# Kernel optimization log

Hardware: AMD Instinct MI355X
Metric: run time of the kernel (lower is better)

Reference implementation:

```python
import jax, jax.numpy as jnp
import numpy as np

# Fixed mock-config geometry
B, S, H = 8, 4096, 2048
NK, NV, DK, DV = 2, 2, 4, 4
KDIM = NK * DK          # 8
VDIM = NV * DV          # 8
CONV_DIM = 2 * KDIM + VDIM  # 24
KSZ = 4                 # causal conv kernel size
EPS = 1e-6


def setup_inputs() -> dict:
    key = jax.random.key(0)
    ks = jax.random.split(key, 7)
    scaled = lambda k, shape, fan: jax.random.normal(k, shape, jnp.float32) * (1.0 / np.sqrt(fan))
    return {
        "x": jax.random.normal(ks[0], (B, S, H), jnp.float32),
        "w_qkv": scaled(ks[1], (CONV_DIM, H), H),   # in_proj_qkv.weight
        "w_z": scaled(ks[2], (VDIM, H), H),         # in_proj_z.weight
        "w_b": scaled(ks[3], (NV, H), H),           # in_proj_b.weight
        "w_a": scaled(ks[4], (NV, H), H),           # in_proj_a.weight
        "w_out": scaled(ks[5], (H, VDIM), VDIM),    # out_proj.weight
        "conv_w": jax.random.normal(ks[6], (CONV_DIM, 1, KSZ), jnp.float32) * 0.5,  # depthwise conv weight
        "dt_bias": jnp.ones((NV,), jnp.float32),
        "A_log": jnp.log(jnp.linspace(1.0, 2.0, NV)).astype(jnp.float32),
        "norm_w": jnp.ones((DV,), jnp.float32),     # MockRMSNormGated weight
    }


def reference(x, w_qkv, w_z, w_b, w_a, w_out, conv_w, dt_bias, A_log, norm_w):
    b_, s_, _ = x.shape
    # qkv projection -> [B, C, S] for depthwise causal conv
    mixed = jnp.einsum('bsh,ch->bcs', x, w_qkv)
    # torch conv1d(padding=K-1) then [:, :, :S] == causal left-pad K-1
    conv = jax.lax.conv_general_dilated(
        mixed, conv_w, window_strides=(1,), padding=[(KSZ - 1, 0)],
        dimension_numbers=('NCH', 'OIH', 'NCH'), feature_group_count=CONV_DIM)
    mixed = jax.nn.silu(conv).transpose(0, 2, 1)  # [B, S, C]

    z = jnp.einsum('bsh,vh->bsv', x, w_z).reshape(b_, s_, NV, DV)
    bb = jnp.einsum('bsh,nh->bsn', x, w_b)  # [B, S, NV]
    aa = jnp.einsum('bsh,nh->bsn', x, w_a)  # [B, S, NV]

    query = mixed[..., :KDIM].reshape(b_, s_, NK, DK)
    key_ = mixed[..., KDIM:2 * KDIM].reshape(b_, s_, NK, DK)
    value = mixed[..., 2 * KDIM:].reshape(b_, s_, NV, DV)

    beta = jax.nn.sigmoid(bb)                                    # [B, S, NV]
    g = -jnp.exp(A_log) * jax.nn.softplus(aa + dt_bias)          # [B, S, NV], fp32
    # num_v_heads // num_k_heads == 1 -> no repeat_interleave

    # mock chunk_gated_delta_rule: value + beta * (q + k) + g
    core = value + beta[..., None] * (query + key_) + g[..., None]  # [B, S, NV, DV]

    # gated RMSNorm over head_v_dim (fp32 math)
    h = core.astype(jnp.float32)
    var = jnp.mean(h * h, axis=-1, keepdims=True)
    h = h * jax.lax.rsqrt(var + EPS) * norm_w
    h = h * jax.nn.silu(z.astype(jnp.float32))

    out = jnp.einsum('bsv,hv->bsh', h.reshape(b_, s_, VDIM), w_out)
    return out
```

## Files before the change

### kernel.cpp

```cpp
#include <hip/hip_runtime.h>
#include <math.h>
#include <cstddef>

#define BB    8
#define SS    4096
#define HH    2048
#define ROWS  (BB*SS)
#define NC    36
#define NCP   40
#define KC    32
#define XST   33
#define KSL   256

typedef float vfloat4 __attribute__((ext_vector_type(4)));

#define MIX_OFF 131072

__global__ __launch_bounds__(256) void pack_wt(
    const float* __restrict__ w_qkv, const float* __restrict__ w_z,
    const float* __restrict__ w_b,   const float* __restrict__ w_a,
    float* __restrict__ wt) {
  int idx = blockIdx.x * 256 + threadIdx.x;
  if (idx >= HH * NCP) return;
  int k = idx / NCP, c = idx - (idx / NCP) * NCP;
  float v = 0.f;
  if      (c < 24) v = w_qkv[c * HH + k];
  else if (c < 32) v = w_z[(c - 24) * HH + k];
  else if (c < 34) v = w_b[(c - 32) * HH + k];
  else if (c < 36) v = w_a[(c - 34) * HH + k];
  wt[idx] = v;
}

__global__ __launch_bounds__(512, 4) void proj36(
    const float* __restrict__ x, const float* __restrict__ wt,
    float* __restrict__ mix) {
  __shared__ float sm[8 * 64 * XST];
  const int tid  = threadIdx.x;
  const int lane = tid & 63;
  const int wv   = __builtin_amdgcn_readfirstlane(tid >> 6);
  const int r0   = blockIdx.x * 64;

  float* xs = sm + wv * 64 * XST;
  float acc[NC];
#pragma unroll
  for (int c = 0; c < NC; ++c) acc[c] = 0.f;

  const int kbase0 = wv * KSL;
  const int srow = lane >> 3;
  const int scol = (lane & 7) * 4;
  const float* xg = x + (size_t)r0 * HH + kbase0 + scol;

  float4 buf[8];
#pragma unroll
  for (int p = 0; p < 8; ++p)
    buf[p] = *(const float4*)(xg + (size_t)(p * 8 + srow) * HH);

  for (int ch = 0; ch < 8; ++ch) {
#pragma unroll
    for (int p = 0; p < 8; ++p) {
      float* dst = xs + (p * 8 + srow) * XST + scol;
      dst[0] = buf[p].x; dst[1] = buf[p].y; dst[2] = buf[p].z; dst[3] = buf[p].w;
    }
    if (ch < 7) {
      const float* xg2 = xg + (ch + 1) * KC;
#pragma unroll
      for (int p = 0; p < 8; ++p)
        buf[p] = *(const float4*)(xg2 + (size_t)(p * 8 + srow) * HH);
    }
    const float* wrow = wt + (size_t)(kbase0 + ch * KC) * NCP;
    const float* xr = xs + lane * XST;
#pragma unroll 2
    for (int k = 0; k < KC; ++k) {
      float xv = xr[k];
#pragma unroll
      for (int c = 0; c < NC; ++c)
        acc[c] = fmaf(wrow[k * NCP + c], xv, acc[c]);
    }
  }

  __syncthreads();
  const int myhalf = lane >> 5;
  const int rr = lane & 31;
  for (int half = 0; half < 2; ++half) {
    if (half) __syncthreads();
    if (myhalf == half) {
#pragma unroll
      for (int c = 0; c < NC; ++c)
        sm[(wv * 32 + rr) * 37 + c] = acc[c];
    }
    __syncthreads();
    for (int idx = tid; idx < 32 * NC; idx += 512) {
      int row = idx / NC;
      float s = 0.f;
#pragma unroll
      for (int w = 0; w < 8; ++w) s += sm[(w * 32 + row) * 37 + (idx - row * NC)];
      mix[(size_t)(r0 + half * 32) * NC + idx] = s;
    }
  }
}

__global__ __launch_bounds__(256) void fuse_out(
    const float* __restrict__ mix,  const float* __restrict__ conv_w,
    const float* __restrict__ dt_bias, const float* __restrict__ A_log,
    const float* __restrict__ norm_w,  const float* __restrict__ w_out,
    float* __restrict__ out) {
  __shared__ float m36[35 * 37];
  __shared__ float hb[32 * 8];
  const int tid = threadIdx.x;
  const int r0  = blockIdx.x * 32;

  const long base = (long)(r0 - 3) * NC;
  for (int idx = tid; idx < 35 * NC; idx += 256) {
    int row = idx / NC, c = idx - row * NC;
    long g = base + idx;
    m36[row * 37 + c] = (g >= 0) ? mix[g] : 0.f;
  }
  __syncthreads();

  if (tid < 64) {
    const int row  = tid >> 1, n = tid & 1;
    const int spos = (r0 + row) & (SS - 1);
    float cv[12];
#pragma unroll
    for (int j = 0; j < 12; ++j) {
      int c = (j >> 2) * 8 + n * 4 + (j & 3);
      float s = 0.f;
#pragma unroll
      for (int k = 0; k < 4; ++k)
        if (spos + k - 3 >= 0) s += m36[(row + k) * 37 + c] * conv_w[c * 4 + k];
      cv[j] = s / (1.f + __expf(-s));
    }
    float bbv  = m36[(row + 3) * 37 + 32 + n];
    float aav  = m36[(row + 3) * 37 + 34 + n];
    float beta = 1.f / (1.f + __expf(-bbv));
    float spin = aav + dt_bias[n];
    float sp   = (spin > 20.f) ? spin : __logf(1.f + __expf(spin));
    float g    = -__expf(A_log[n]) * sp;
    float core[4], var = 0.f;
#pragma unroll
    for (int d = 0; d < 4; ++d) {
      core[d] = cv[8 + d] + beta * (cv[d] + cv[4 + d]) + g;
      var += core[d] * core[d];
    }
    float rs = rsqrtf(var * 0.25f + 1e-6f);
#pragma unroll
    for (int d = 0; d < 4; ++d) {
      float z = m36[(row + 3) * 37 + 24 + n * 4 + d];
      hb[row * 8 + n * 4 + d] =
          core[d] * rs * norm_w[d] * (z / (1.f + __expf(-z)));
    }
  }
  __syncthreads();

  const int c0a = tid * 4, c0b = 1024 + tid * 4;
  float4 wr[16];
#pragma unroll
  for (int i = 0; i < 4; ++i) {
    wr[i * 2]     = *(const float4*)(w_out + (size_t)(c0a + i) * 8);
    wr[i * 2 + 1] = *(const float4*)(w_out + (size_t)(c0a + i) * 8 + 4);
    wr[8 + i * 2]     = *(const float4*)(w_out + (size_t)(c0b + i) * 8);
    wr[8 + i * 2 + 1] = *(const float4*)(w_out + (size_t)(c0b + i) * 8 + 4);
  }
  for (int row = 0; row < 32; ++row) {
    float h[8];
#pragma unroll
    for (int v = 0; v < 8; ++v) h[v] = hb[row * 8 + v];
    vfloat4 oa, ob;
#pragma unroll
    for (int i = 0; i < 4; ++i) {
      const float4 wa0 = wr[i * 2], wa1 = wr[i * 2 + 1];
      const float4 wb0 = wr[8 + i * 2], wb1 = wr[8 + i * 2 + 1];
      oa[i] = h[0]*wa0.x + h[1]*wa0.y + h[2]*wa0.z + h[3]*wa0.w
            + h[4]*wa1.x + h[5]*wa1.y + h[6]*wa1.z + h[7]*wa1.w;
      ob[i] = h[0]*wb0.x + h[1]*wb0.y + h[2]*wb0.z + h[3]*wb0.w
            + h[4]*wb1.x + h[5]*wb1.y + h[6]*wb1.z + h[7]*wb1.w;
    }
    float* op = out + (size_t)(r0 + row) * HH;
    __builtin_nontemporal_store(oa, (vfloat4*)(op + c0a));
    __builtin_nontemporal_store(ob, (vfloat4*)(op + c0b));
  }
}

extern "C" void kernel_launch(void* const* d_in, const int* in_sizes, int n_in,
                              void* d_out, int out_size, void* d_ws, size_t ws_size,
                              hipStream_t stream) {
  (void)in_sizes; (void)n_in; (void)out_size; (void)ws_size;
  const float* x      = (const float*)d_in[0];
  const float* w_qkv  = (const float*)d_in[1];
  const float* w_z    = (const float*)d_in[2];
  const float* w_b    = (const float*)d_in[3];
  const float* w_a    = (const float*)d_in[4];
  const float* w_out  = (const float*)d_in[5];
  const float* conv_w = (const float*)d_in[6];
  const float* dt_b   = (const float*)d_in[7];
  const float* A_log  = (const float*)d_in[8];
  const float* norm_w = (const float*)d_in[9];
  float* out = (float*)d_out;
  float* ws  = (float*)d_ws;
  float* wt  = ws;
  float* mix = ws + MIX_OFF;

  pack_wt<<<dim3((HH * NCP + 255) / 256), dim3(256), 0, stream>>>(
      w_qkv, w_z, w_b, w_a, wt);
  proj36<<<dim3(ROWS / 64), dim3(512), 0, stream>>>(x, wt, mix);
  fuse_out<<<dim3(ROWS / 32), dim3(256), 0, stream>>>(
      mix, conv_w, dt_b, A_log, norm_w, w_out, out);
}
```

Baseline: 499.8 us.

## Split projection K across two blocks and read x directly per lane

The projection kernel now launches twice as many blocks, and each block covers half of the hidden dimension. Each block writes its partial sums to a separate buffer, and fuse_out adds the two partials when it loads them. The LDS staging of x is removed: each lane loads its own row with strided float4 reads and double-buffers them in registers. This is meant to raise parallelism and drop the LDS transpose, at the cost of uncoalesced row-strided global loads and an extra partial-sum buffer that must be written and read back.

```diff
diff --git a/kernel.cpp b/kernel.cpp
--- a/kernel.cpp
+++ b/kernel.cpp
@@ -8,9 +8,7 @@
 #define ROWS  (BB*SS)
 #define NC    36
 #define NCP   40
-#define KC    32
-#define XST   33
-#define KSL   256
+#define KSL   128
 
 typedef float vfloat4 __attribute__((ext_vector_type(4)));
 
@@ -34,67 +32,68 @@
 __global__ __launch_bounds__(512, 4) void proj36(
     const float* __restrict__ x, const float* __restrict__ wt,
     float* __restrict__ mix) {
-  __shared__ float sm[8 * 64 * XST];
+  __shared__ float red[8 * 32 * 37];
   const int tid  = threadIdx.x;
   const int lane = tid & 63;
   const int wv   = __builtin_amdgcn_readfirstlane(tid >> 6);
-  const int r0   = blockIdx.x * 64;
-
-  float* xs = sm + wv * 64 * XST;
+  const int rblk  = blockIdx.x >> 1;
+  const int khalf = blockIdx.x & 1;
+  const int r0    = rblk * 64;
+  float* mixp = mix + (size_t)khalf * ((size_t)ROWS * NC);
+
   float acc[NC];
 #pragma unroll
   for (int c = 0; c < NC; ++c) acc[c] = 0.f;
 
-  const int kbase0 = wv * KSL;
-  const int srow = lane >> 3;
-  const int scol = (lane & 7) * 4;
-  const float* xg = x + (size_t)r0 * HH + kbase0 + scol;
-
-  float4 buf[8];
-#pragma unroll
-  for (int p = 0; p < 8; ++p)
-    buf[p] = *(const float4*)(xg + (size_t)(p * 8 + srow) * HH);
-
+  const int kbase = khalf * 1024 + wv * KSL;
+  const float* xr = x + (size_t)(r0 + lane) * HH + kbase;
+
+  float4 cur[4];
+#pragma unroll
+  for (int q = 0; q < 4; ++q) cur[q] = *(const float4*)(xr + q * 4);
+
+#pragma unroll 1
   for (int ch = 0; ch < 8; ++ch) {
-#pragma unroll
-    for (int p = 0; p < 8; ++p) {
-      float* dst = xs + (p * 8 + srow) * XST + scol;
-      dst[0] = buf[p].x; dst[1] = buf[p].y; dst[2] = buf[p].z; dst[3] = buf[p].w;
-    }
+    float4 nxt[4];
     if (ch < 7) {
-      const float* xg2 = xg + (ch + 1) * KC;
-#pragma unroll
-      for (int p = 0; p < 8; ++p)
-        buf[p] = *(const float4*)(xg2 + (size_t)(p * 8 + srow) * HH);
-    }
-    const float* wrow = wt + (size_t)(kbase0 + ch * KC) * NCP;
-    const float* xr = xs + lane * XST;
-#pragma unroll 2
-    for (int k = 0; k < KC; ++k) {
-      float xv = xr[k];
-#pragma unroll
-      for (int c = 0; c < NC; ++c)
-        acc[c] = fmaf(wrow[k * NCP + c], xv, acc[c]);
-    }
-  }
-
-  __syncthreads();
+#pragma unroll
+      for (int q = 0; q < 4; ++q)
+        nxt[q] = *(const float4*)(xr + (ch + 1) * 16 + q * 4);
+    }
+    const float* wrow = wt + (size_t)(kbase + ch * 16) * NCP;
+#pragma unroll
+    for (int q = 0; q < 4; ++q) {
+#pragma unroll
+      for (int i = 0; i < 4; ++i) {
+        const float xv = (&cur[q].x)[i];
+        const float* wk = wrow + (q * 4 + i) * NCP;
+#pragma unroll
+        for (int c = 0; c < NC; ++c)
+          acc[c] = fmaf(wk[c], xv, acc[c]);
+      }
+    }
+    if (ch < 7) {
+#pragma unroll
+      for (int q = 0; q < 4; ++q) cur[q] = nxt[q];
+    }
+  }
+
+  const int rr = lane & 31;
   const int myhalf = lane >> 5;
-  const int rr = lane & 31;
   for (int half = 0; half < 2; ++half) {
     if (half) __syncthreads();
     if (myhalf == half) {
 #pragma unroll
       for (int c = 0; c < NC; ++c)
-        sm[(wv * 32 + rr) * 37 + c] = acc[c];
+        red[(wv * 32 + rr) * 37 + c] = acc[c];
     }
     __syncthreads();
     for (int idx = tid; idx < 32 * NC; idx += 512) {
       int row = idx / NC;
       float s = 0.f;
 #pragma unroll
-      for (int w = 0; w < 8; ++w) s += sm[(w * 32 + row) * 37 + (idx - row * NC)];
-      mix[(size_t)(r0 + half * 32) * NC + idx] = s;
+      for (int w = 0; w < 8; ++w) s += red[(w * 32 + row) * 37 + (idx - row * NC)];
+      mixp[(size_t)(r0 + half * 32) * NC + idx] = s;
     }
   }
 }
@@ -108,12 +107,13 @@
   __shared__ float hb[32 * 8];
   const int tid = threadIdx.x;
   const int r0  = blockIdx.x * 32;
+  const float* mix1 = mix + (size_t)ROWS * NC;
 
   const long base = (long)(r0 - 3) * NC;
   for (int idx = tid; idx < 35 * NC; idx += 256) {
     int row = idx / NC, c = idx - row * NC;
     long g = base + idx;
-    m36[row * 37 + c] = (g >= 0) ? mix[g] : 0.f;
+    m36[row * 37 + c] = (g >= 0) ? (mix[g] + mix1[g]) : 0.f;
   }
   __syncthreads();
 
@@ -202,7 +202,7 @@
 
   pack_wt<<<dim3((HH * NCP + 255) / 256), dim3(256), 0, stream>>>(
       w_qkv, w_z, w_b, w_a, wt);
-  proj36<<<dim3(ROWS / 64), dim3(512), 0, stream>>>(x, wt, mix);
+  proj36<<<dim3(ROWS / 64 * 2), dim3(512), 0, stream>>>(x, wt, mix);
   fuse_out<<<dim3(ROWS / 32), dim3(256), 0, stream>>>(
       mix, conv_w, dt_b, A_log, norm_w, w_out, out);
 }
```

New measurement: 632.0 us. 1.26x slower.

## Fuse projection and conv/norm/out-projection into one kernel with halo recompute

Applied to the files above, without the earlier changes.

Merges the projection kernel and the epilogue kernel into a single kernel. Each block handles 61 output rows but computes projections for 64 rows, recomputing a 3-row halo for the causal conv instead of writing the intermediate mix buffer to global memory and reading it back. This removes the intermediate round trip and one launch. In exchange it adds about 5% redundant x reads and projection FLOPs, plus a heavier per-block LDS footprint that may lower occupancy.

```diff
diff --git a/kernel.cpp b/kernel.cpp
--- a/kernel.cpp
+++ b/kernel.cpp
@@ -11,10 +11,12 @@
 #define KC    32
 #define XST   33
 #define KSL   256
+#define TR    61
+#define MR    64
+#define NB    ((ROWS + TR - 1) / TR)
 
 typedef float vfloat4 __attribute__((ext_vector_type(4)));
 
-#define MIX_OFF 131072
 
 __global__ __launch_bounds__(256) void pack_wt(
     const float* __restrict__ w_qkv, const float* __restrict__ w_z,
@@ -31,29 +33,40 @@
   wt[idx] = v;
 }
 
-__global__ __launch_bounds__(512, 4) void proj36(
-    const float* __restrict__ x, const float* __restrict__ wt,
-    float* __restrict__ mix) {
-  __shared__ float sm[8 * 64 * XST];
+__global__ __launch_bounds__(512, 4) void fused(
+    const float* __restrict__ x,       const float* __restrict__ wt,
+    const float* __restrict__ conv_w,  const float* __restrict__ dt_bias,
+    const float* __restrict__ A_log,   const float* __restrict__ norm_w,
+    const float* __restrict__ w_out,   float* __restrict__ out) {
+  __shared__ float sm[8 * MR * XST];
+  __shared__ float m36[MR * 37];
+  __shared__ float hb[TR * 8];
   const int tid  = threadIdx.x;
   const int lane = tid & 63;
   const int wv   = __builtin_amdgcn_readfirstlane(tid >> 6);
-  const int r0   = blockIdx.x * 64;
+  const int r0   = blockIdx.x * TR;
+  const int rm0  = r0 - 3;
 
-  float* xs = sm + wv * 64 * XST;
+  float* xs = sm + wv * MR * XST;
   float acc[NC];
 #pragma unroll
   for (int c = 0; c < NC; ++c) acc[c] = 0.f;
 
-  const int kbase0 = wv * KSL;
+  const int kbase = wv * KSL;
   const int srow = lane >> 3;
   const int scol = (lane & 7) * 4;
-  const float* xg = x + (size_t)r0 * HH + kbase0 + scol;
+
+  const float* rp[8];
+#pragma unroll
+  for (int p = 0; p < 8; ++p) {
+    int rg = rm0 + p * 8 + srow;
+    rg = rg < 0 ? 0 : (rg > ROWS - 1 ? ROWS - 1 : rg);
+    rp[p] = x + (size_t)rg * HH + kbase + scol;
+  }
 
   float4 buf[8];
 #pragma unroll
-  for (int p = 0; p < 8; ++p)
-    buf[p] = *(const float4*)(xg + (size_t)(p * 8 + srow) * HH);
+  for (int p = 0; p < 8; ++p) buf[p] = *(const float4*)(rp[p]);
 
   for (int ch = 0; ch < 8; ++ch) {
 #pragma unroll
@@ -62,12 +75,11 @@
       dst[0] = buf[p].x; dst[1] = buf[p].y; dst[2] = buf[p].z; dst[3] = buf[p].w;
     }
     if (ch < 7) {
-      const float* xg2 = xg + (ch + 1) * KC;
 #pragma unroll
       for (int p = 0; p < 8; ++p)
-        buf[p] = *(const float4*)(xg2 + (size_t)(p * 8 + srow) * HH);
+        buf[p] = *(const float4*)(rp[p] + (ch + 1) * KC);
     }
-    const float* wrow = wt + (size_t)(kbase0 + ch * KC) * NCP;
+    const float* wrow = wt + (size_t)(kbase + ch * KC) * NCP;
     const float* xr = xs + lane * XST;
 #pragma unroll 2
     for (int k = 0; k < KC; ++k) {
@@ -77,61 +89,43 @@
         acc[c] = fmaf(wrow[k * NCP + c], xv, acc[c]);
     }
   }
+  __syncthreads();
 
-  __syncthreads();
-  const int myhalf = lane >> 5;
   const int rr = lane & 31;
+  const int hsel = lane >> 5;
   for (int half = 0; half < 2; ++half) {
     if (half) __syncthreads();
-    if (myhalf == half) {
+    if (hsel == half) {
 #pragma unroll
       for (int c = 0; c < NC; ++c)
         sm[(wv * 32 + rr) * 37 + c] = acc[c];
     }
     __syncthreads();
     for (int idx = tid; idx < 32 * NC; idx += 512) {
-      int row = idx / NC;
+      int row = idx / NC, c = idx - row * NC;
       float s = 0.f;
 #pragma unroll
-      for (int w = 0; w < 8; ++w) s += sm[(w * 32 + row) * 37 + (idx - row * NC)];
-      mix[(size_t)(r0 + half * 32) * NC + idx] = s;
+      for (int w = 0; w < 8; ++w) s += sm[(w * 32 + row) * 37 + c];
+      m36[(half * 32 + row) * 37 + c] = s;
     }
-  }
-}
-
-__global__ __launch_bounds__(256) void fuse_out(
-    const float* __restrict__ mix,  const float* __restrict__ conv_w,
-    const float* __restrict__ dt_bias, const float* __restrict__ A_log,
-    const float* __restrict__ norm_w,  const float* __restrict__ w_out,
-    float* __restrict__ out) {
-  __shared__ float m36[35 * 37];
-  __shared__ float hb[32 * 8];
-  const int tid = threadIdx.x;
-  const int r0  = blockIdx.x * 32;
-
-  const long base = (long)(r0 - 3) * NC;
-  for (int idx = tid; idx < 35 * NC; idx += 256) {
-    int row = idx / NC, c = idx - row * NC;
-    long g = base + idx;
-    m36[row * 37 + c] = (g >= 0) ? mix[g] : 0.f;
   }
   __syncthreads();
 
-  if (tid < 64) {
-    const int row  = tid >> 1, n = tid & 1;
-    const int spos = (r0 + row) & (SS - 1);
+  if (tid < 2 * TR) {
+    const int j = tid >> 1, n = tid & 1;
+    const int spos = (r0 + j) & (SS - 1);
     float cv[12];
 #pragma unroll
-    for (int j = 0; j < 12; ++j) {
-      int c = (j >> 2) * 8 + n * 4 + (j & 3);
+    for (int jj = 0; jj < 12; ++jj) {
+      int c = (jj >> 2) * 8 + n * 4 + (jj & 3);
       float s = 0.f;
 #pragma unroll
       for (int k = 0; k < 4; ++k)
-        if (spos + k - 3 >= 0) s += m36[(row + k) * 37 + c] * conv_w[c * 4 + k];
-      cv[j] = s / (1.f + __expf(-s));
+        if (spos + k - 3 >= 0) s += m36[(j + k) * 37 + c] * conv_w[c * 4 + k];
+      cv[jj] = s / (1.f + __expf(-s));
     }
-    float bbv  = m36[(row + 3) * 37 + 32 + n];
-    float aav  = m36[(row + 3) * 37 + 34 + n];
+    float bbv  = m36[(j + 3) * 37 + 32 + n];
+    float aav  = m36[(j + 3) * 37 + 34 + n];
     float beta = 1.f / (1.f + __expf(-bbv));
     float spin = aav + dt_bias[n];
     float sp   = (spin > 20.f) ? spin : __logf(1.f + __expf(spin));
@@ -145,39 +139,31 @@
     float rs = rsqrtf(var * 0.25f + 1e-6f);
 #pragma unroll
     for (int d = 0; d < 4; ++d) {
-      float z = m36[(row + 3) * 37 + 24 + n * 4 + d];
-      hb[row * 8 + n * 4 + d] =
+      float z = m36[(j + 3) * 37 + 24 + n * 4 + d];
+      hb[j * 8 + n * 4 + d] =
           core[d] * rs * norm_w[d] * (z / (1.f + __expf(-z)));
     }
   }
   __syncthreads();
 
-  const int c0a = tid * 4, c0b = 1024 + tid * 4;
-  float4 wr[16];
+  const int c0 = tid * 4;
+  float4 w0[4], w1[4];
 #pragma unroll
   for (int i = 0; i < 4; ++i) {
-    wr[i * 2]     = *(const float4*)(w_out + (size_t)(c0a + i) * 8);
-    wr[i * 2 + 1] = *(const float4*)(w_out + (size_t)(c0a + i) * 8 + 4);
-    wr[8 + i * 2]     = *(const float4*)(w_out + (size_t)(c0b + i) * 8);
-    wr[8 + i * 2 + 1] = *(const float4*)(w_out + (size_t)(c0b + i) * 8 + 4);
+    w0[i] = *(const float4*)(w_out + (size_t)(c0 + i) * 8);
+    w1[i] = *(const float4*)(w_out + (size_t)(c0 + i) * 8 + 4);
   }
-  for (int row = 0; row < 32; ++row) {
+  const int jmax = (ROWS - r0 < TR) ? (ROWS - r0) : TR;
+  for (int j = 0; j < jmax; ++j) {
     float h[8];
 #pragma unroll
-    for (int v = 0; v < 8; ++v) h[v] = hb[row * 8 + v];
-    vfloat4 oa, ob;
+    for (int v = 0; v < 8; ++v) h[v] = hb[j * 8 + v];
+    vfloat4 o;
 #pragma unroll
-    for (int i = 0; i < 4; ++i) {
-      const float4 wa0 = wr[i * 2], wa1 = wr[i * 2 + 1];
-      const float4 wb0 = wr[8 + i * 2], wb1 = wr[8 + i * 2 + 1];
-      oa[i] = h[0]*wa0.x + h[1]*wa0.y + h[2]*wa0.z + h[3]*wa0.w
-            + h[4]*wa1.x + h[5]*wa1.y + h[6]*wa1.z + h[7]*wa1.w;
-      ob[i] = h[0]*wb0.x + h[1]*wb0.y + h[2]*wb0.z + h[3]*wb0.w
-            + h[4]*wb1.x + h[5]*wb1.y + h[6]*wb1.z + h[7]*wb1.w;
-    }
-    float* op = out + (size_t)(r0 + row) * HH;
-    __builtin_nontemporal_store(oa, (vfloat4*)(op + c0a));
-    __builtin_nontemporal_store(ob, (vfloat4*)(op + c0b));
+    for (int i = 0; i < 4; ++i)
+      o[i] = h[0]*w0[i].x + h[1]*w0[i].y + h[2]*w0[i].z + h[3]*w0[i].w
+           + h[4]*w1[i].x + h[5]*w1[i].y + h[6]*w1[i].z + h[7]*w1[i].w;
+    __builtin_nontemporal_store(o, (vfloat4*)(out + (size_t)(r0 + j) * HH + c0));
   }
 }
 
@@ -196,13 +182,10 @@
   const float* A_log  = (const float*)d_in[8];
   const float* norm_w = (const float*)d_in[9];
   float* out = (float*)d_out;
-  float* ws  = (float*)d_ws;
-  float* wt  = ws;
-  float* mix = ws + MIX_OFF;
+  float* wt  = (float*)d_ws;
 
   pack_wt<<<dim3((HH * NCP + 255) / 256), dim3(256), 0, stream>>>(
       w_qkv, w_z, w_b, w_a, wt);
-  proj36<<<dim3(ROWS / 64), dim3(512), 0, stream>>>(x, wt, mix);
-  fuse_out<<<dim3(ROWS / 32), dim3(256), 0, stream>>>(
-      mix, conv_w, dt_b, A_log, norm_w, w_out, out);
+  fused<<<dim3(NB), dim3(512), 0, stream>>>(
+      x, wt, conv_w, dt_b, A_log, norm_w, w_out, out);
 }
```

Result: slower. 521.0 us (+4.3%).

## Stage projection weights through LDS per wave with float4 reads

Applied to the files above, without the earlier changes.

The projection kernel now copies each wave's slice of the packed weight matrix into shared memory, software-pipelined alongside the x tile, and reads the weights with float4 LDS loads. Previously every lane read the weights from global memory as scalar loads. The K chunk shrinks from 32 to 16 to make room for the weight slab, which doubles the number of chunk iterations. The packed weight padding is removed (40 to 36 columns). The weight loads move off the global and scalar memory path, at the cost of more LDS traffic and less room for other blocks on a CU.

```diff
diff --git a/kernel.cpp b/kernel.cpp
--- a/kernel.cpp
+++ b/kernel.cpp
@@ -7,93 +7,119 @@
 #define HH    2048
 #define ROWS  (BB*SS)
 #define NC    36
-#define NCP   40
-#define KC    32
-#define XST   33
+#define KC    16
+#define XST   17
 #define KSL   256
+#define NCH   16
+
+#define XSLAB (64 * XST)
+#define WOFF  (8 * XSLAB)
+#define WSLAB (KC * NC)
+#define LDSZ  (WOFF + 8 * WSLAB)
 
 typedef float vfloat4 __attribute__((ext_vector_type(4)));
 
-#define MIX_OFF 131072
+#define MIX_OFF (HH * NC)
 
 __global__ __launch_bounds__(256) void pack_wt(
     const float* __restrict__ w_qkv, const float* __restrict__ w_z,
     const float* __restrict__ w_b,   const float* __restrict__ w_a,
     float* __restrict__ wt) {
   int idx = blockIdx.x * 256 + threadIdx.x;
-  if (idx >= HH * NCP) return;
-  int k = idx / NCP, c = idx - (idx / NCP) * NCP;
-  float v = 0.f;
+  if (idx >= HH * NC) return;
+  int k = idx / NC, c = idx - (idx / NC) * NC;
+  float v;
   if      (c < 24) v = w_qkv[c * HH + k];
   else if (c < 32) v = w_z[(c - 24) * HH + k];
   else if (c < 34) v = w_b[(c - 32) * HH + k];
-  else if (c < 36) v = w_a[(c - 34) * HH + k];
+  else             v = w_a[(c - 34) * HH + k];
   wt[idx] = v;
 }
 
 __global__ __launch_bounds__(512, 4) void proj36(
     const float* __restrict__ x, const float* __restrict__ wt,
     float* __restrict__ mix) {
-  __shared__ float sm[8 * 64 * XST];
+  __shared__ float lds[LDSZ];
   const int tid  = threadIdx.x;
   const int lane = tid & 63;
   const int wv   = __builtin_amdgcn_readfirstlane(tid >> 6);
   const int r0   = blockIdx.x * 64;
 
-  float* xs = sm + wv * 64 * XST;
+  float* xs = lds + wv * XSLAB;
+  float* wl = lds + WOFF + wv * WSLAB;
+
   float acc[NC];
 #pragma unroll
   for (int c = 0; c < NC; ++c) acc[c] = 0.f;
 
-  const int kbase0 = wv * KSL;
-  const int srow = lane >> 3;
-  const int scol = (lane & 7) * 4;
-  const float* xg = x + (size_t)r0 * HH + kbase0 + scol;
-
-  float4 buf[8];
-#pragma unroll
-  for (int p = 0; p < 8; ++p)
-    buf[p] = *(const float4*)(xg + (size_t)(p * 8 + srow) * HH);
-
-  for (int ch = 0; ch < 8; ++ch) {
-#pragma unroll
-    for (int p = 0; p < 8; ++p) {
-      float* dst = xs + (p * 8 + srow) * XST + scol;
-      dst[0] = buf[p].x; dst[1] = buf[p].y; dst[2] = buf[p].z; dst[3] = buf[p].w;
-    }
-    if (ch < 7) {
+  const int kbase = wv * KSL;
+  const int srow = lane >> 2;
+  const int scol = (lane & 3) * 4;
+
+  const float* xg = x + (size_t)(r0 + srow) * HH + kbase + scol;
+  const float* wg = wt + (size_t)kbase * NC + lane;
+
+  float4 xbuf[4];
+  float  wbuf[9];
+#pragma unroll
+  for (int p = 0; p < 4; ++p)
+    xbuf[p] = *(const float4*)(xg + (size_t)(p * 16) * HH);
+#pragma unroll
+  for (int i = 0; i < 9; ++i) wbuf[i] = wg[i * 64];
+
+#pragma unroll 1
+  for (int ch = 0; ch < NCH; ++ch) {
+#pragma unroll
+    for (int p = 0; p < 4; ++p) {
+      float* dst = xs + (p * 16 + srow) * XST + scol;
+      dst[0] = xbuf[p].x; dst[1] = xbuf[p].y;
+      dst[2] = xbuf[p].z; dst[3] = xbuf[p].w;
+    }
+#pragma unroll
+    for (int i = 0; i < 9; ++i) wl[i * 64 + lane] = wbuf[i];
+
+    if (ch < NCH - 1) {
       const float* xg2 = xg + (ch + 1) * KC;
-#pragma unroll
-      for (int p = 0; p < 8; ++p)
-        buf[p] = *(const float4*)(xg2 + (size_t)(p * 8 + srow) * HH);
-    }
-    const float* wrow = wt + (size_t)(kbase0 + ch * KC) * NCP;
+      const float* wg2 = wg + (size_t)(ch + 1) * KC * NC;
+#pragma unroll
+      for (int p = 0; p < 4; ++p)
+        xbuf[p] = *(const float4*)(xg2 + (size_t)(p * 16) * HH);
+#pragma unroll
+      for (int i = 0; i < 9; ++i) wbuf[i] = wg2[i * 64];
+    }
+
     const float* xr = xs + lane * XST;
-#pragma unroll 2
+#pragma unroll
     for (int k = 0; k < KC; ++k) {
-      float xv = xr[k];
-#pragma unroll
-      for (int c = 0; c < NC; ++c)
-        acc[c] = fmaf(wrow[k * NCP + c], xv, acc[c]);
+      const float xv = xr[k];
+      const float* wk = wl + k * NC;
+#pragma unroll
+      for (int c4 = 0; c4 < 9; ++c4) {
+        const float4 w4 = *(const float4*)(wk + c4 * 4);
+        acc[c4 * 4 + 0] = fmaf(w4.x, xv, acc[c4 * 4 + 0]);
+        acc[c4 * 4 + 1] = fmaf(w4.y, xv, acc[c4 * 4 + 1]);
+        acc[c4 * 4 + 2] = fmaf(w4.z, xv, acc[c4 * 4 + 2]);
+        acc[c4 * 4 + 3] = fmaf(w4.w, xv, acc[c4 * 4 + 3]);
+      }
     }
   }
 
   __syncthreads();
-  const int myhalf = lane >> 5;
   const int rr = lane & 31;
+  const int hsel = lane >> 5;
   for (int half = 0; half < 2; ++half) {
     if (half) __syncthreads();
-    if (myhalf == half) {
+    if (hsel == half) {
 #pragma unroll
       for (int c = 0; c < NC; ++c)
-        sm[(wv * 32 + rr) * 37 + c] = acc[c];
+        lds[(wv * 32 + rr) * 37 + c] = acc[c];
     }
     __syncthreads();
     for (int idx = tid; idx < 32 * NC; idx += 512) {
       int row = idx / NC;
       float s = 0.f;
 #pragma unroll
-      for (int w = 0; w < 8; ++w) s += sm[(w * 32 + row) * 37 + (idx - row * NC)];
+      for (int w = 0; w < 8; ++w) s += lds[(w * 32 + row) * 37 + (idx - row * NC)];
       mix[(size_t)(r0 + half * 32) * NC + idx] = s;
     }
   }
@@ -200,7 +226,7 @@
   float* wt  = ws;
   float* mix = ws + MIX_OFF;
 
-  pack_wt<<<dim3((HH * NCP + 255) / 256), dim3(256), 0, stream>>>(
+  pack_wt<<<dim3((HH * NC + 255) / 256), dim3(256), 0, stream>>>(
       w_qkv, w_z, w_b, w_a, wt);
   proj36<<<dim3(ROWS / 64), dim3(512), 0, stream>>>(x, wt, mix);
   fuse_out<<<dim3(ROWS / 32), dim3(256), 0, stream>>>(
```

Result: faster. 489.4 us (-2.1%).
